# Performance work log

Hardware: AMD Instinct MI355X
Metric: run time of the kernel (lower is better)

## Reference

```python
import jax, jax.numpy as jnp
import numpy as np
from jax import lax

S, B, W = 128, 64, 16          # sent_len, batch, word_len
V, CV = 50000, 100             # word vocab, char vocab
WE, CE, FN, CK = 300, 30, 4, 3 # word emb dim, char emb dim, char filter num, char kernel
C = 512                        # cnn_out_channel
NT = 20                        # number of tags
NL = 3                         # number of GLU conv layers
PAD = 0


def setup_inputs() -> dict:
    key = jax.random.key(0)
    ks = jax.random.split(key, 16)
    words = jax.random.randint(ks[0], (S, B), 1, V)          # no pads -> full CRF mask
    chars = jax.random.randint(ks[1], (B, S, W), 1, CV)
    tags = jax.random.randint(ks[2], (S, B), 0, NT)
    word_emb = jax.random.normal(ks[3], (V, WE), jnp.float32) * 0.1
    char_emb = jax.random.normal(ks[4], (CV, CE), jnp.float32) * 0.1
    char_cnn_w = jax.random.normal(ks[5], (CE * FN, 1, CK), jnp.float32) * 0.1  # grouped conv, groups=CE
    char_cnn_b = jax.random.normal(ks[6], (CE * FN,), jnp.float32) * 0.01
    lin_w = jax.random.normal(ks[7], (WE + CE * FN, C), jnp.float32) * 0.05
    lin_b = jax.random.normal(ks[8], (C,), jnp.float32) * 0.01
    conv_w = jax.random.normal(ks[9], (NL, 2 * C, C, 3), jnp.float32) * 0.03
    conv_b = jax.random.normal(ks[10], (NL, 2 * C), jnp.float32) * 0.01
    fc_w = jax.random.normal(ks[11], (C, NT), jnp.float32) * 0.05
    fc_b = jax.random.normal(ks[12], (NT,), jnp.float32) * 0.01
    crf_start = jax.random.normal(ks[13], (NT,), jnp.float32) * 0.1
    crf_end = jax.random.normal(ks[14], (NT,), jnp.float32) * 0.1
    crf_trans = jax.random.normal(ks[15], (NT, NT), jnp.float32) * 0.1
    return dict(words=words, chars=chars, tags=tags, word_emb=word_emb, char_emb=char_emb,
                char_cnn_w=char_cnn_w, char_cnn_b=char_cnn_b, lin_w=lin_w, lin_b=lin_b,
                conv_w=conv_w, conv_b=conv_b, fc_w=fc_w, fc_b=fc_b,
                crf_start=crf_start, crf_end=crf_end, crf_trans=crf_trans)


def _emissions(words, chars, word_emb, char_emb, char_cnn_w, char_cnn_b,
               lin_w, lin_b, conv_w, conv_b, fc_w, fc_b):
    s, b = words.shape
    # word embeddings: [S,B,WE]
    emb_out = word_emb[words]
    # char embeddings + batched grouped char-CNN (replaces the python loop over sent positions)
    ch = char_emb[chars]                                   # [B,S,W,CE]
    ch = ch.reshape(b * s, W, CE).transpose(0, 2, 1)       # [B*S, CE, W]
    co = lax.conv_general_dilated(ch, char_cnn_w, (1,), 'VALID',
                                  dimension_numbers=('NCH', 'OIH', 'NCH'),
                                  feature_group_count=CE)
    co = co + char_cnn_b[None, :, None]                    # [B*S, CE*FN, W-CK+1]
    cf = co.max(axis=2).reshape(b, s, CE * FN).transpose(1, 0, 2)  # [S,B,120]
    word_features = jnp.concatenate([emb_out, cf], axis=2)  # [S,B,420]
    # gated-CNN (GLU) encoder
    h = word_features @ lin_w + lin_b                      # [S,B,C]
    h = jnp.transpose(h, (1, 2, 0))                        # [B,C,S]
    scale = jnp.sqrt(jnp.asarray(0.5, h.dtype))
    for l in range(conv_w.shape[0]):
        c = lax.conv_general_dilated(h, conv_w[l], (1,), ((1, 1),),
                                     dimension_numbers=('NCH', 'OIH', 'NCH'))
        c = c + conv_b[l][None, :, None]                   # [B,2C,S]
        a, g = jnp.split(c, 2, axis=1)
        h = (a * jax.nn.sigmoid(g) + h) * scale            # GLU + residual + scale
    enc = jnp.transpose(h, (2, 0, 1))                      # [S,B,C]
    emis = enc @ fc_w + fc_b                               # [S,B,NT]
    mask = (words != PAD)                                  # [S,B]
    return emis, mask


def _crf_nll(emis, tags, mask, crf_start, crf_end, crf_trans):
    s, b, nt = emis.shape
    maskf = mask.astype(emis.dtype)
    bi = jnp.arange(b)
    # numerator: score of the gold path
    emis_sc = jnp.take_along_axis(emis, tags[:, :, None], axis=2)[..., 0]  # [S,B]
    trans_sc = crf_trans[tags[:-1], tags[1:]]                              # [S-1,B]
    num = crf_start[tags[0]] + emis_sc[0] + ((trans_sc + emis_sc[1:]) * maskf[1:]).sum(0)
    last_idx = mask.sum(0).astype(jnp.int32) - 1
    num = num + crf_end[tags[last_idx, bi]]
    # denominator: forward algorithm (sequential DP over time)
    alpha0 = crf_start[None, :] + emis[0]                  # [B,NT]
    def step(alpha, xs):
        e_t, m_t = xs
        nxt = jax.nn.logsumexp(alpha[:, :, None] + crf_trans[None] + e_t[:, None, :], axis=1)
        return jnp.where(m_t[:, None], nxt, alpha), None
    alpha, _ = lax.scan(step, alpha0, (emis[1:], mask[1:]))
    logz = jax.nn.logsumexp(alpha + crf_end[None, :], axis=1)
    return -(num - logz).sum()


def _viterbi(emis, mask, crf_start, crf_end, crf_trans):
    s, b, nt = emis.shape
    bi = jnp.arange(b)
    ident = jnp.broadcast_to(jnp.arange(nt)[None, :], (b, nt))
    score0 = crf_start[None, :] + emis[0]                  # [B,NT]
    def step(score, xs):
        e_t, m_t = xs
        brd = score[:, :, None] + crf_trans[None]          # [B,NT_prev,NT_cur]
        bp = jnp.argmax(brd, axis=1)                       # [B,NT]
        nxt = jnp.max(brd, axis=1) + e_t
        score = jnp.where(m_t[:, None], nxt, score)
        bp = jnp.where(m_t[:, None], bp, ident)
        return score, bp
    final, bps = lax.scan(step, score0, (emis[1:], mask[1:]))  # bps [S-1,B,NT]
    last_tag = jnp.argmax(final + crf_end[None, :], axis=1)    # [B]
    def back(tag, bp):
        prev = bp[bi, tag]
        return prev, tag
    first_tag, rest = lax.scan(back, last_tag, bps, reverse=True)  # rest: tags at 1..S-1
    return jnp.concatenate([first_tag[None], rest], axis=0).astype(jnp.int32)  # [S,B]


def reference(words, chars, tags, word_emb, char_emb, char_cnn_w, char_cnn_b,
              lin_w, lin_b, conv_w, conv_b, fc_w, fc_b, crf_start, crf_end, crf_trans):
    emis, mask = _emissions(words, chars, word_emb, char_emb, char_cnn_w, char_cnn_b,
                            lin_w, lin_b, conv_w, conv_b, fc_w, fc_b)
    crf_out = _viterbi(emis, mask, crf_start, crf_end, crf_trans)
    crf_loss = _crf_nll(emis, tags, mask, crf_start, crf_end, crf_trans)
    return crf_out, crf_loss
```

## Files before the change

kernel.cpp:

```cpp
#include <hip/hip_runtime.h>
#include <math.h>

typedef unsigned short ushort_t;
typedef short bf16x8 __attribute__((ext_vector_type(8)));
typedef float f32x4 __attribute__((ext_vector_type(4)));
typedef unsigned short u16x8 __attribute__((ext_vector_type(8)));

#define S_ 128
#define B_ 64
#define W_ 16
#define CE_ 30
#define FN_ 4
#define WE_ 300
#define FEAT_ 420
#define C_ 512
#define NT_ 20
#define KL_ 448

#define LOG2E_ 1.44269504088896340736f
#define LN2_   0.69314718055994530942f

#define WF_OFF   0
#define EM_OFF   3440640
#define NLL_OFF  3604480
#define H0_OFF   3604608
#define HBUF_F   2129920
#define H1_OFF   (H0_OFF + HBUF_F)
#define WS_OFF   (H1_OFF + HBUF_F)
#define WSP_F    2359296
#define LW_OFF   (WS_OFF + WSP_F)
#define FS_OFF   (LW_OFF + 114688)
#define FW_OFF   (FS_OFF + 1835008)
#define WLAYER   (1024*1536)

__device__ __forceinline__ float b2f(ushort_t h) {
    unsigned u = ((unsigned)h) << 16;
    float f; __builtin_memcpy(&f, &u, 4); return f;
}
__device__ __forceinline__ ushort_t f2b(float f) {
    unsigned u; __builtin_memcpy(&u, &f, 4);
    unsigned r = (u + 0x7FFFu + ((u >> 16) & 1u)) >> 16;
    return (ushort_t)r;
}
__device__ __forceinline__ void gload16(const void* g, void* l) {
    __builtin_amdgcn_global_load_lds((const __attribute__((address_space(1))) void*)g,
                                     (__attribute__((address_space(3))) void*)l,
                                     16, 0, 0);
}

__global__ void k_word_gather(const int* __restrict__ words,
                              const float* __restrict__ word_emb,
                              float* __restrict__ wf) {
    int n = blockIdx.x;
    int wid = words[n];
    int t = threadIdx.x;
    if (t < WE_ / 4) {
        const float4* src = (const float4*)(word_emb + (size_t)wid * WE_);
        float4* dst = (float4*)(wf + (size_t)n * FEAT_);
        dst[t] = src[t];
    }
}

__global__ void k_char_cnn(const int* __restrict__ chars,
                           const float* __restrict__ char_emb,
                           const float* __restrict__ cw,
                           const float* __restrict__ cb,
                           float* __restrict__ wf) {
    int n = blockIdx.x;
    int b = n >> 7;
    int s = n & 127;
    __shared__ int cidx[W_];
    int t = threadIdx.x;
    if (t < W_) cidx[t] = chars[n * W_ + t];
    __syncthreads();
    if (t < CE_ * FN_) {
        int g = t >> 2;
        float w0 = cw[t*3+0], w1 = cw[t*3+1], w2 = cw[t*3+2];
        float x[W_];
        #pragma unroll
        for (int j = 0; j < W_; ++j) x[j] = char_emb[cidx[j] * CE_ + g];
        float m = -INFINITY;
        #pragma unroll
        for (int j = 0; j < W_ - 2; ++j) {
            float v = x[j]*w0 + x[j+1]*w1 + x[j+2]*w2;
            m = fmaxf(m, v);
        }
        wf[(size_t)(s * B_ + b) * FEAT_ + WE_ + t] = m + cb[t];
    }
}

__global__ void k_split_w(const float* __restrict__ conv_w,
                          ushort_t* __restrict__ Wt) {
    size_t i = (size_t)blockIdx.x * 256 + threadIdx.x;
    int ci = (int)(i & 511);
    int kr = (int)((i >> 9) % 3);
    size_t lo_ = i / 1536;
    Wt[i] = f2b(conv_w[lo_ * 1536 + (size_t)ci * 3 + kr]);
}

__global__ void k_split_lw(const float* __restrict__ lin_w,
                           ushort_t* __restrict__ Lh) {
    int k = blockIdx.x;
    int c = threadIdx.x;
    float v = (k < FEAT_) ? lin_w[(size_t)k * C_ + c] : 0.f;
    Lh[(size_t)c * KL_ + k] = f2b(v);
}

__global__ void k_split_wf(const float* __restrict__ wf,
                           ushort_t* __restrict__ Fh) {
    int np = blockIdx.x;
    int b = np >> 7, s = np & 127;
    const float* src = wf + (size_t)(s * B_ + b) * FEAT_;
    int t = threadIdx.x;
    #pragma unroll
    for (int r = 0; r < 2; ++r) {
        int k = t + r * 224;
        float v = (k < FEAT_) ? src[k] : 0.f;
        Fh[(size_t)np * KL_ + k] = f2b(v);
    }
}

__global__ void k_split_fw(const float* __restrict__ fc_w, float* __restrict__ fwT) {
    int idx = blockIdx.x * 256 + threadIdx.x;
    if (idx < NT_ * C_) {
        int j = idx >> 9, c = idx & 511;
        fwT[idx] = fc_w[(size_t)c * NT_ + j];
    }
}

__global__ void k_zero_pad(ushort_t* b0, ushort_t* b1) {
    ushort_t* buf = blockIdx.y ? b1 : b0;
    int b = blockIdx.x;
    int t = threadIdx.x;
    unsigned* r0 = (unsigned*)(buf + ((size_t)b * 130 + 0) * 512);
    unsigned* r1 = (unsigned*)(buf + ((size_t)b * 130 + 129) * 512);
    r0[t] = 0u; r1[t] = 0u;
}

__global__ __launch_bounds__(256) void k_lin_gemm(
    const ushort_t* __restrict__ Lh, const ushort_t* __restrict__ Fh,
    const float* __restrict__ lb, ushort_t* __restrict__ Oh)
{
    __shared__ short lds[8192];
    short* AhS = lds;
    short* BhS = lds + 4096;

    const int bid = blockIdx.x;
    const int c0 = (bid & 3) << 7;
    const int n0 = (bid >> 2) << 7;
    const int t = threadIdx.x;
    const int w = t >> 6;
    const int lane = t & 63;
    const int wr = w >> 1, wc = w & 1;

    const int srow0 = (w << 5) + (lane >> 2);
    const int srow1 = srow0 + 16;
    const int j0 = (lane & 3) ^ ((srow0 >> 1) & 3);
    const int j1 = (lane & 3) ^ ((srow1 >> 1) & 3);
    const size_t aoff0 = (size_t)(c0 + srow0) * KL_ + j0 * 8;
    const size_t aoff1 = (size_t)(c0 + srow1) * KL_ + j1 * 8;
    const size_t boff0 = (size_t)(n0 + srow0) * KL_ + j0 * 8;
    const size_t boff1 = (size_t)(n0 + srow1) * KL_ + j1 * 8;
    const int wofs = w << 10;

    const int lr = lane & 15, kg = lane >> 4;
    int aro[4], bro[4];
    #pragma unroll
    for (int m = 0; m < 4; ++m) { int r = (wr << 6) + (m << 4) + lr; aro[m] = (r << 5) + ((kg ^ ((r >> 1) & 3)) << 3); }
    #pragma unroll
    for (int n = 0; n < 4; ++n) { int r = (wc << 6) + (n << 4) + lr; bro[n] = (r << 5) + ((kg ^ ((r >> 1) & 3)) << 3); }

    f32x4 acc[4][4];
    #pragma unroll
    for (int m = 0; m < 4; ++m)
        #pragma unroll
        for (int n = 0; n < 4; ++n) acc[m][n] = (f32x4){0.f, 0.f, 0.f, 0.f};

    for (int k0 = 0; k0 < KL_; k0 += 32) {
        gload16(Lh + aoff0 + k0, AhS + wofs);
        gload16(Lh + aoff1 + k0, AhS + wofs + 512);
        gload16(Fh + boff0 + k0, BhS + wofs);
        gload16(Fh + boff1 + k0, BhS + wofs + 512);
        __syncthreads();
        bf16x8 avh[4], bvh[4];
        #pragma unroll
        for (int m = 0; m < 4; ++m) avh[m] = *(const bf16x8*)(AhS + aro[m]);
        #pragma unroll
        for (int n = 0; n < 4; ++n) bvh[n] = *(const bf16x8*)(BhS + bro[n]);
        #pragma unroll
        for (int m = 0; m < 4; ++m)
            #pragma unroll
            for (int n = 0; n < 4; ++n)
                acc[m][n] = __builtin_amdgcn_mfma_f32_16x16x32_bf16(avh[m], bvh[n], acc[m][n], 0, 0, 0);
        __syncthreads();
    }

    #pragma unroll
    for (int m = 0; m < 4; ++m) {
        const int c = c0 + (wr << 6) + (m << 4) + (kg << 2);
        float4 bb = *(const float4*)(lb + c);
        #pragma unroll
        for (int n = 0; n < 4; ++n) {
            const int np = n0 + (wc << 6) + (n << 4) + lr;
            const int b = np >> 7, s = np & 127;
            ushort4 h4;
            h4.x = f2b(acc[m][n][0] + bb.x);
            h4.y = f2b(acc[m][n][1] + bb.y);
            h4.z = f2b(acc[m][n][2] + bb.z);
            h4.w = f2b(acc[m][n][3] + bb.w);
            *(ushort4*)(Oh + ((size_t)b * 130 + s + 1) * 512 + c) = h4;
        }
    }
}

__global__ __launch_bounds__(256) void k_conv_gemm(
    const ushort_t* __restrict__ Wt, const ushort_t* __restrict__ Ht,
    const float* __restrict__ cb,
    ushort_t* __restrict__ Ot)
{
    __shared__ short lds[17408];
    short* AS = lds;
    short* BS = lds + 12288;
    float* g_lds = (float*)lds;

    const int bid  = blockIdx.x;
    const int co0  = (bid & 7) << 6;
    const int b    = bid >> 3;
    const int t    = threadIdx.x;
    const int w    = t >> 6;
    const int lane = t & 63;
    const int wr   = w >> 1;
    const int wc   = w & 1;

    const int srow0 = (w << 5) + (lane >> 2);
    const int srow1 = srow0 + 16;
    const int j0 = (lane & 3) ^ ((srow0 >> 1) & 3);
    const int j1 = (lane & 3) ^ ((srow1 >> 1) & 3);
    const int coA0 = (srow0 < 64) ? (co0 + srow0) : (512 + co0 + srow0 - 64);
    const int coA1 = (srow1 < 64) ? (co0 + srow1) : (512 + co0 + srow1 - 64);
    const size_t aoff0 = (size_t)coA0 * 1536 + j0 * 8;
    const size_t aoff1 = (size_t)coA1 * 1536 + j1 * 8;
    const int lrow = lane >> 2;
    const int wofs = w << 10;

    const int lr = lane & 15, kg = lane >> 4;
    int aro[4];
    #pragma unroll
    for (int m = 0; m < 4; ++m) { int r = (wr << 6) + (m << 4) + lr; aro[m] = (r << 5) + ((kg ^ ((r >> 1) & 3)) << 3); }
    int bro[3][4];
    #pragma unroll
    for (int kr = 0; kr < 3; ++kr)
        #pragma unroll
        for (int n = 0; n < 4; ++n) {
            int r = (wc << 6) + (n << 4) + lr + kr;
            bro[kr][n] = (r << 5) + ((kg ^ ((r >> 1) & 3)) << 3);
        }

    f32x4 acc[4][4];
    #pragma unroll
    for (int m = 0; m < 4; ++m)
        #pragma unroll
        for (int n = 0; n < 4; ++n) acc[m][n] = (f32x4){0.f, 0.f, 0.f, 0.f};

    for (int ci0 = 0; ci0 < 512; ci0 += 32) {
        #pragma unroll
        for (int kr = 0; kr < 3; ++kr) {
            gload16(Wt + aoff0 + kr * 512 + ci0, AS + kr * 4096 + wofs);
            gload16(Wt + aoff1 + kr * 512 + ci0, AS + kr * 4096 + wofs + 512);
        }
        for (int i = w; i < 9; i += 4) {
            const int rr = (i << 4) + lrow;
            const int sl = (lane & 3) ^ ((rr >> 1) & 3);
            gload16(Ht + ((size_t)b * 130 + rr) * 512 + ci0 + sl * 8, BS + (i << 9));
        }
        __syncthreads();
        #pragma unroll
        for (int kr = 0; kr < 3; ++kr) {
            const short* A_h = AS + kr * 4096;
            bf16x8 avh[4], bvh[4];
            #pragma unroll
            for (int m = 0; m < 4; ++m) avh[m] = *(const bf16x8*)(A_h + aro[m]);
            #pragma unroll
            for (int n = 0; n < 4; ++n) bvh[n] = *(const bf16x8*)(BS + bro[kr][n]);
            #pragma unroll
            for (int m = 0; m < 4; ++m)
                #pragma unroll
                for (int n = 0; n < 4; ++n)
                    acc[m][n] = __builtin_amdgcn_mfma_f32_16x16x32_bf16(avh[m], bvh[n], acc[m][n], 0, 0, 0);
        }
        __syncthreads();
    }

    const float rs = 0.70710678118654752f;
    if (wr == 1) {
        #pragma unroll
        for (int m = 0; m < 4; ++m) {
            const int co_l = (m << 4) + (kg << 2);
            float4 bg = *(const float4*)(cb + 512 + co0 + co_l);
            #pragma unroll
            for (int n = 0; n < 4; ++n) {
                const int s_l = (wc << 6) + (n << 4) + lr;
                float4 gv;
                gv.x = acc[m][n][0] + bg.x;
                gv.y = acc[m][n][1] + bg.y;
                gv.z = acc[m][n][2] + bg.z;
                gv.w = acc[m][n][3] + bg.w;
                *(float4*)&g_lds[s_l * 68 + co_l] = gv;
            }
        }
    }
    __syncthreads();
    if (wr == 0) {
        #pragma unroll
        for (int m = 0; m < 4; ++m) {
            const int co_l = (m << 4) + (kg << 2);
            float4 ba = *(const float4*)(cb + co0 + co_l);
            #pragma unroll
            for (int n = 0; n < 4; ++n) {
                const int s_l = (wc << 6) + (n << 4) + lr;
                float4 gv = *(const float4*)&g_lds[s_l * 68 + co_l];
                size_t dst = ((size_t)b * 130 + s_l + 1) * 512 + co0 + co_l;
                ushort4 rh = *(const ushort4*)(Ht + dst);
                float a0 = acc[m][n][0] + ba.x, g0 = gv.x;
                float a1 = acc[m][n][1] + ba.y, g1 = gv.y;
                float a2 = acc[m][n][2] + ba.z, g2 = gv.z;
                float a3 = acc[m][n][3] + ba.w, g3 = gv.w;
                ushort4 h4;
                h4.x = f2b((a0 / (1.f + expf(-g0)) + b2f(rh.x)) * rs);
                h4.y = f2b((a1 / (1.f + expf(-g1)) + b2f(rh.y)) * rs);
                h4.z = f2b((a2 / (1.f + expf(-g2)) + b2f(rh.z)) * rs);
                h4.w = f2b((a3 / (1.f + expf(-g3)) + b2f(rh.w)) * rs);
                *(ushort4*)(Ot + dst) = h4;
            }
        }
    }
}

__global__ __launch_bounds__(256) void k_emis3(const ushort_t* __restrict__ hh,
                                               const float* __restrict__ fwT,
                                               const float* __restrict__ fc_b,
                                               float* __restrict__ emis) {
    __shared__ short hlds[16 * 520];
    __shared__ float wlds[20 * 516];
    const int b  = blockIdx.y;
    const int sc = blockIdx.x;
    const int t  = threadIdx.x;
    const int w  = t >> 6, lane = t & 63;

    #pragma unroll
    for (int i = 0; i < 4; ++i) {
        int r = w * 4 + i;
        gload16(hh + ((size_t)b * 130 + sc * 16 + r + 1) * 512 + lane * 8,
                hlds + r * 520);
    }
    for (int idx = t; idx < 20 * 128; idx += 256) {
        int j = idx >> 7, cq = (idx & 127) << 2;
        *(float4*)&wlds[j * 516 + cq] = *(const float4*)(fwT + j * 512 + cq);
    }
    __syncthreads();

    #pragma unroll
    for (int pass = 0; pass < 2; ++pass) {
        int slot = t + pass * 256;
        if (slot < 16 * NT_) {
            int r = slot / NT_, j = slot - r * NT_;
            const short* hp = hlds + r * 520;
            const float* wp = wlds + j * 516;
            float acc = 0.f;
            for (int c0 = 0; c0 < 512; c0 += 8) {
                u16x8 hv = *(const u16x8*)(hp + c0);
                float4 w0 = *(const float4*)(wp + c0);
                float4 w1 = *(const float4*)(wp + c0 + 4);
                acc += b2f(hv[0])*w0.x + b2f(hv[1])*w0.y + b2f(hv[2])*w0.z + b2f(hv[3])*w0.w
                     + b2f(hv[4])*w1.x + b2f(hv[5])*w1.y + b2f(hv[6])*w1.z + b2f(hv[7])*w1.w;
            }
            int s = sc * 16 + r;
            emis[((size_t)s * B_ + b) * NT_ + j] = acc + fc_b[j];
        }
    }
}

#define VMAX(a, b) __builtin_elementwise_max((a), (b))
#define MAX20T(mx, a0, a1, a2, a3, a4) \
    { f32x4 mv_ = VMAX(VMAX(VMAX(a0, a1), VMAX(a2, a3)), a4); \
      mx = fmaxf(fmaxf(mv_[0], mv_[1]), fmaxf(mv_[2], mv_[3])); }
#define SEL(ov, oi, av, ai, bv2, bi2) \
    { bool g_ = (bv2) > (av); ov = g_ ? (bv2) : (av); oi = g_ ? (bi2) : (ai); }

__global__ __launch_bounds__(128) void k_crf(const float* __restrict__ emis,
                                             const int* __restrict__ words,
                                             const int* __restrict__ tags,
                                             const float* __restrict__ tstart,
                                             const float* __restrict__ tend,
                                             const float* __restrict__ ttrans,
                                             float* __restrict__ nll,
                                             float* __restrict__ out) {
    __shared__ float e_lds[S_ * NT_];
    __shared__ float pe_lds[S_ * NT_];
    __shared__ int   bp_lds[(S_ - 1) * NT_];
    __shared__ float alphaL[32];
    __shared__ float scoreL[32];
    const int b = blockIdx.x;
    const int t = threadIdx.x;

    for (int idx = t; idx < S_ * NT_; idx += 128) {
        int tt = idx / NT_, j = idx - tt * NT_;
        float ev = emis[((size_t)tt * B_ + b) * NT_ + j];
        e_lds[idx] = ev;
        pe_lds[idx] = __builtin_amdgcn_exp2f(ev * LOG2E_);
    }
    __syncthreads();

    const int ln = t & 63;
    unsigned long long mlo = __ballot(words[ln * B_ + b] != 0);
    unsigned long long mhi = __ballot(words[(64 + ln) * B_ + b] != 0);
    const bool act = ln < NT_;
    const int jc = act ? ln : 0;
    f32x4 t0, t1, t2, t3, t4;
    #define LDTC(v, q) v = (f32x4){ ttrans[(4*(q)+0)*NT_ + jc], ttrans[(4*(q)+1)*NT_ + jc], \
                                    ttrans[(4*(q)+2)*NT_ + jc], ttrans[(4*(q)+3)*NT_ + jc] }
    LDTC(t0, 0); LDTC(t1, 1); LDTC(t2, 2); LDTC(t3, 3); LDTC(t4, 4);

    if (t < 64) {
        float part = 0.f;
        for (int tt = ln; tt < S_; tt += 64) {
            int tgc = tags[tt * B_ + b];
            bool m = ((tt < 64 ? (mlo >> tt) : (mhi >> (tt - 64))) & 1ull) != 0;
            if (tt == 0) {
                part += tstart[tgc] + e_lds[tgc];
            } else if (m) {
                int tgp = tags[(tt - 1) * B_ + b];
                part += ttrans[tgp * NT_ + tgc] + e_lds[tt * NT_ + tgc];
            }
        }
        #pragma unroll
        for (int o = 32; o >= 1; o >>= 1) part += __shfl_down(part, o);

        f32x4 E0, E1, E2, E3, E4;
        #define EXPC(d, s) d[0]=__builtin_amdgcn_exp2f(s[0]*LOG2E_); d[1]=__builtin_amdgcn_exp2f(s[1]*LOG2E_); \
                           d[2]=__builtin_amdgcn_exp2f(s[2]*LOG2E_); d[3]=__builtin_amdgcn_exp2f(s[3]*LOG2E_)
        EXPC(E0, t0); EXPC(E1, t1); EXPC(E2, t2); EXPC(E3, t3); EXPC(E4, t4);

        float a0own = tstart[jc] + e_lds[jc];
        if (act) alphaL[ln] = a0own;
        asm volatile("s_waitcnt lgkmcnt(0)" ::: "memory");
        f32x4 a0 = *(const f32x4*)&alphaL[0];
        f32x4 a1 = *(const f32x4*)&alphaL[4];
        f32x4 a2 = *(const f32x4*)&alphaL[8];
        f32x4 a3 = *(const f32x4*)&alphaL[12];
        f32x4 a4 = *(const f32x4*)&alphaL[16];
        float m0; MAX20T(m0, a0, a1, a2, a3, a4);
        float beta = __builtin_amdgcn_exp2f((a0own - m0) * LOG2E_);
        int L2 = 0;
        for (int tt = 1; tt < S_; ++tt) {
            bool m = ((tt < 64 ? (mlo >> tt) : (mhi >> (tt - 64))) & 1ull) != 0;
            if (m) {
                float pe = pe_lds[tt * NT_ + jc];
                if (act) alphaL[ln] = beta;
                asm volatile("s_waitcnt lgkmcnt(0)" ::: "memory");
                f32x4 b0 = *(const f32x4*)&alphaL[0];
                f32x4 b1 = *(const f32x4*)&alphaL[4];
                f32x4 b2 = *(const f32x4*)&alphaL[8];
                f32x4 b3 = *(const f32x4*)&alphaL[12];
                f32x4 b4 = *(const f32x4*)&alphaL[16];
                float mx; MAX20T(mx, b0, b1, b2, b3, b4);
                f32x4 pr = b0 * E0 + b1 * E1 + b2 * E2 + b3 * E3 + b4 * E4;
                float dot = (pr[0] + pr[1]) + (pr[2] + pr[3]);
                unsigned bits; __builtin_memcpy(&bits, &mx, 4);
                int ex = (int)((bits >> 23) & 255u) - 127;
                unsigned rb = (unsigned)(127 - ex) << 23;
                float r; __builtin_memcpy(&r, &rb, 4);
                L2 += ex;
                beta = dot * r * pe;
            }
        }
        if (act) alphaL[ln] = beta;
        asm volatile("s_waitcnt lgkmcnt(0)" ::: "memory");
        f32x4 b0 = *(const f32x4*)&alphaL[0];
        f32x4 b1 = *(const f32x4*)&alphaL[4];
        f32x4 b2 = *(const f32x4*)&alphaL[8];
        f32x4 b3 = *(const f32x4*)&alphaL[12];
        f32x4 b4 = *(const f32x4*)&alphaL[16];
        #define LDE(v, q) v = (f32x4){ tend[4*(q)+0], tend[4*(q)+1], tend[4*(q)+2], tend[4*(q)+3] }
        f32x4 d0, d1, d2, d3, d4;
        LDE(d0, 0); LDE(d1, 1); LDE(d2, 2); LDE(d3, 3); LDE(d4, 4);
        f32x4 n0, n1, n2, n3, n4;
        EXPC(n0, d0); EXPC(n1, d1); EXPC(n2, d2); EXPC(n3, d3); EXPC(n4, d4);
        f32x4 pr = b0 * n0 + b1 * n1 + b2 * n2 + b3 * n3 + b4 * n4;
        float sm = (pr[0] + pr[1]) + (pr[2] + pr[3]);
        float logz = m0 + ((float)L2 + __builtin_amdgcn_logf(sm)) * LN2_;
        if (ln == 0) {
            int cnt = __popcll(mlo) + __popcll(mhi);
            float num = part + tend[tags[(cnt - 1) * B_ + b]];
            nll[b] = logz - num;
        }
    } else {
        float sown = tstart[jc] + e_lds[jc];
        if (act) scoreL[ln] = sown;
        asm volatile("s_waitcnt lgkmcnt(0)" ::: "memory");
        for (int tt = 1; tt < S_; ++tt) {
            float e = e_lds[tt * NT_ + jc];
            f32x4 a0 = *(const f32x4*)&scoreL[0];
            f32x4 a1 = *(const f32x4*)&scoreL[4];
            f32x4 a2 = *(const f32x4*)&scoreL[8];
            f32x4 a3 = *(const f32x4*)&scoreL[12];
            f32x4 a4 = *(const f32x4*)&scoreL[16];
            f32x4 v0 = a0 + t0, v1 = a1 + t1, v2 = a2 + t2, v3 = a3 + t3, v4 = a4 + t4;
            float p0v, p1v, p2v, p3v, p4v, p5v, p6v, p7v, p8v, p9v;
            int   p0i, p1i, p2i, p3i, p4i, p5i, p6i, p7i, p8i, p9i;
            SEL(p0v, p0i, v0[0], 0,  v0[1], 1);
            SEL(p1v, p1i, v0[2], 2,  v0[3], 3);
            SEL(p2v, p2i, v1[0], 4,  v1[1], 5);
            SEL(p3v, p3i, v1[2], 6,  v1[3], 7);
            SEL(p4v, p4i, v2[0], 8,  v2[1], 9);
            SEL(p5v, p5i, v2[2], 10, v2[3], 11);
            SEL(p6v, p6i, v3[0], 12, v3[1], 13);
            SEL(p7v, p7i, v3[2], 14, v3[3], 15);
            SEL(p8v, p8i, v4[0], 16, v4[1], 17);
            SEL(p9v, p9i, v4[2], 18, v4[3], 19);
            float q0v, q1v, q2v, q3v, q4v; int q0i, q1i, q2i, q3i, q4i;
            SEL(q0v, q0i, p0v, p0i, p1v, p1i);
            SEL(q1v, q1i, p2v, p2i, p3v, p3i);
            SEL(q2v, q2i, p4v, p4i, p5v, p5i);
            SEL(q3v, q3i, p6v, p6i, p7v, p7i);
            SEL(q4v, q4i, p8v, p8i, p9v, p9i);
            float r0v, r1v; int r0i, r1i;
            SEL(r0v, r0i, q0v, q0i, q1v, q1i);
            SEL(r1v, r1i, q2v, q2i, q3v, q3i);
            float s0v; int s0i;
            SEL(s0v, s0i, r0v, r0i, r1v, r1i);
            float best; int bi;
            SEL(best, bi, s0v, s0i, q4v, q4i);
            bool m = ((tt < 64 ? (mlo >> tt) : (mhi >> (tt - 64))) & 1ull) != 0;
            float nxt = best + e;
            sown = m ? nxt : sown;
            if (act) {
                scoreL[ln] = sown;
                bp_lds[(tt - 1) * NT_ + ln] = m ? bi : ln;
            }
            asm volatile("s_waitcnt lgkmcnt(0)" ::: "memory");
        }
        if (ln == 0) {
            f32x4 a0 = *(const f32x4*)&scoreL[0];
            f32x4 a1 = *(const f32x4*)&scoreL[4];
            f32x4 a2 = *(const f32x4*)&scoreL[8];
            f32x4 a3 = *(const f32x4*)&scoreL[12];
            f32x4 a4 = *(const f32x4*)&scoreL[16];
            f32x4 d0 = (f32x4){ tend[0],  tend[1],  tend[2],  tend[3]  };
            f32x4 d1 = (f32x4){ tend[4],  tend[5],  tend[6],  tend[7]  };
            f32x4 d2 = (f32x4){ tend[8],  tend[9],  tend[10], tend[11] };
            f32x4 d3 = (f32x4){ tend[12], tend[13], tend[14], tend[15] };
            f32x4 d4 = (f32x4){ tend[16], tend[17], tend[18], tend[19] };
            f32x4 v0 = a0 + d0, v1 = a1 + d1, v2 = a2 + d2, v3 = a3 + d3, v4 = a4 + d4;
            float p0v, p1v, p2v, p3v, p4v, p5v, p6v, p7v, p8v, p9v;
            int   p0i, p1i, p2i, p3i, p4i, p5i, p6i, p7i, p8i, p9i;
            SEL(p0v, p0i, v0[0], 0,  v0[1], 1);
            SEL(p1v, p1i, v0[2], 2,  v0[3], 3);
            SEL(p2v, p2i, v1[0], 4,  v1[1], 5);
            SEL(p3v, p3i, v1[2], 6,  v1[3], 7);
            SEL(p4v, p4i, v2[0], 8,  v2[1], 9);
            SEL(p5v, p5i, v2[2], 10, v2[3], 11);
            SEL(p6v, p6i, v3[0], 12, v3[1], 13);
            SEL(p7v, p7i, v3[2], 14, v3[3], 15);
            SEL(p8v, p8i, v4[0], 16, v4[1], 17);
            SEL(p9v, p9i, v4[2], 18, v4[3], 19);
            float q0v, q1v, q2v, q3v, q4v; int q0i, q1i, q2i, q3i, q4i;
            SEL(q0v, q0i, p0v, p0i, p1v, p1i);
            SEL(q1v, q1i, p2v, p2i, p3v, p3i);
            SEL(q2v, q2i, p4v, p4i, p5v, p5i);
            SEL(q3v, q3i, p6v, p6i, p7v, p7i);
            SEL(q4v, q4i, p8v, p8i, p9v, p9i);
            float r0v, r1v; int r0i, r1i;
            SEL(r0v, r0i, q0v, q0i, q1v, q1i);
            SEL(r1v, r1i, q2v, q2i, q3v, q3i);
            float s0v; int s0i;
            SEL(s0v, s0i, r0v, r0i, r1v, r1i);
            float best; int bt;
            SEL(best, bt, s0v, s0i, q4v, q4i);
            int tag = bt;
            for (int tt = S_ - 1; tt >= 1; --tt) {
                out[tt * B_ + b] = (float)tag;
                tag = bp_lds[(tt - 1) * NT_ + tag];
            }
            out[b] = (float)tag;
        }
    }
}

__global__ void k_loss(const float* __restrict__ nll, float* __restrict__ out) {
    float v = nll[threadIdx.x];
    #pragma unroll
    for (int o = 32; o >= 1; o >>= 1) v += __shfl_down(v, o);
    if (threadIdx.x == 0) out[S_ * B_] = v;
}

extern "C" void kernel_launch(void* const* d_in, const int* in_sizes, int n_in,
                              void* d_out, int out_size, void* d_ws, size_t ws_size,
                              hipStream_t stream) {
    (void)in_sizes; (void)n_in; (void)out_size; (void)ws_size;
    const int*   words     = (const int*)d_in[0];
    const int*   chars     = (const int*)d_in[1];
    const int*   tags      = (const int*)d_in[2];
    const float* word_emb  = (const float*)d_in[3];
    const float* char_emb  = (const float*)d_in[4];
    const float* ccw       = (const float*)d_in[5];
    const float* ccb       = (const float*)d_in[6];
    const float* lin_w     = (const float*)d_in[7];
    const float* lin_b     = (const float*)d_in[8];
    const float* conv_w    = (const float*)d_in[9];
    const float* conv_b    = (const float*)d_in[10];
    const float* fc_w      = (const float*)d_in[11];
    const float* fc_b      = (const float*)d_in[12];
    const float* crf_start = (const float*)d_in[13];
    const float* crf_end   = (const float*)d_in[14];
    const float* crf_trans = (const float*)d_in[15];

    float* ws   = (float*)d_ws;
    float* wf   = ws + WF_OFF;
    float* em   = ws + EM_OFF;
    float* nll  = ws + NLL_OFF;
    ushort_t* h0  = (ushort_t*)(ws + H0_OFF);
    ushort_t* h1  = (ushort_t*)(ws + H1_OFF);
    ushort_t* wsp = (ushort_t*)(ws + WS_OFF);
    ushort_t* lwp = (ushort_t*)(ws + LW_OFF);
    ushort_t* fsp = (ushort_t*)(ws + FS_OFF);
    float* fwT  = ws + FW_OFF;
    float* out  = (float*)d_out;

    k_word_gather<<<S_ * B_, 128, 0, stream>>>(words, word_emb, wf);
    k_char_cnn<<<B_ * S_, 128, 0, stream>>>(chars, char_emb, ccw, ccb, wf);
    k_split_w<<<18432, 256, 0, stream>>>(conv_w, wsp);
    k_split_lw<<<KL_, 512, 0, stream>>>(lin_w, lwp);
    k_split_wf<<<S_ * B_, 224, 0, stream>>>(wf, fsp);
    k_split_fw<<<40, 256, 0, stream>>>(fc_w, fwT);
    k_lin_gemm<<<256, 256, 0, stream>>>(lwp, fsp, lin_b, h0);
    k_zero_pad<<<dim3(64, 2), 256, 0, stream>>>(h0, h1);

    k_conv_gemm<<<512, 256, 0, stream>>>(wsp,              h0, conv_b,        h1);
    k_conv_gemm<<<512, 256, 0, stream>>>(wsp + WLAYER,     h1, conv_b + 1024, h0);
    k_conv_gemm<<<512, 256, 0, stream>>>(wsp + 2*WLAYER,   h0, conv_b + 2048, h1);

    k_emis3<<<dim3(8, B_), 256, 0, stream>>>(h1, fwT, fc_b, em);
    k_crf<<<B_, 128, 0, stream>>>(em, words, tags, crf_start, crf_end, crf_trans, nll, out);
    k_loss<<<1, 64, 0, stream>>>(nll, out);
}
```

Before: 217.0 us.

## Split CRF forward and Viterbi recursions into bidirectional halves meeting at midpoint

The CRF kernel now runs four wavefronts per batch element. Forward-alpha and Viterbi-forward cover steps 1..63, while a backward-beta recursion and a backward Viterbi cover steps 127..63. The partition function is combined from the forward and backward vectors at the midpoint, and the Viterbi path is traced outward from the best midpoint tag in both directions. This roughly halves the serial dependency chain length, which was the latency bottleneck, at the cost of more LDS and numerically different log-sum ordering and tie-breaking.

```diff
diff --git a/kernel.cpp b/kernel.cpp
--- a/kernel.cpp
+++ b/kernel.cpp
@@ -386,8 +386,28 @@
       mx = fmaxf(fmaxf(mv_[0], mv_[1]), fmaxf(mv_[2], mv_[3])); }
 #define SEL(ov, oi, av, ai, bv2, bi2) \
     { bool g_ = (bv2) > (av); ov = g_ ? (bv2) : (av); oi = g_ ? (bi2) : (ai); }
-
-__global__ __launch_bounds__(128) void k_crf(const float* __restrict__ emis,
+#define ARGMAX20(best, bi, v0, v1, v2, v3, v4) \
+    { float p0v,p1v,p2v,p3v,p4v,p5v,p6v,p7v,p8v,p9v; \
+      int   p0i,p1i,p2i,p3i,p4i,p5i,p6i,p7i,p8i,p9i; \
+      SEL(p0v,p0i, v0[0],0,  v0[1],1);  SEL(p1v,p1i, v0[2],2,  v0[3],3); \
+      SEL(p2v,p2i, v1[0],4,  v1[1],5);  SEL(p3v,p3i, v1[2],6,  v1[3],7); \
+      SEL(p4v,p4i, v2[0],8,  v2[1],9);  SEL(p5v,p5i, v2[2],10, v2[3],11); \
+      SEL(p6v,p6i, v3[0],12, v3[1],13); SEL(p7v,p7i, v3[2],14, v3[3],15); \
+      SEL(p8v,p8i, v4[0],16, v4[1],17); SEL(p9v,p9i, v4[2],18, v4[3],19); \
+      float q0v,q1v,q2v,q3v,q4v; int q0i,q1i,q2i,q3i,q4i; \
+      SEL(q0v,q0i,p0v,p0i,p1v,p1i); SEL(q1v,q1i,p2v,p2i,p3v,p3i); \
+      SEL(q2v,q2i,p4v,p4i,p5v,p5i); SEL(q3v,q3i,p6v,p6i,p7v,p7i); \
+      SEL(q4v,q4i,p8v,p8i,p9v,p9i); \
+      float r0v,r1v; int r0i,r1i; \
+      SEL(r0v,r0i,q0v,q0i,q1v,q1i); SEL(r1v,r1i,q2v,q2i,q3v,q3i); \
+      float s0v; int s0i; \
+      SEL(s0v,s0i,r0v,r0i,r1v,r1i); \
+      SEL(best,bi,s0v,s0i,q4v,q4i); }
+#define EXPC(d, s) d[0]=__builtin_amdgcn_exp2f(s[0]*LOG2E_); d[1]=__builtin_amdgcn_exp2f(s[1]*LOG2E_); \
+                   d[2]=__builtin_amdgcn_exp2f(s[2]*LOG2E_); d[3]=__builtin_amdgcn_exp2f(s[3]*LOG2E_)
+#define LGKM0() asm volatile("s_waitcnt lgkmcnt(0)" ::: "memory")
+
+__global__ __launch_bounds__(256) void k_crf(const float* __restrict__ emis,
                                              const int* __restrict__ words,
                                              const int* __restrict__ tags,
                                              const float* __restrict__ tstart,
@@ -397,13 +417,17 @@
                                              float* __restrict__ out) {
     __shared__ float e_lds[S_ * NT_];
     __shared__ float pe_lds[S_ * NT_];
-    __shared__ int   bp_lds[(S_ - 1) * NT_];
-    __shared__ float alphaL[32];
-    __shared__ float scoreL[32];
+    __shared__ int   P_lds[S_ * NT_];
+    __shared__ float brA[32], brB[32], brC[32], brD[32];
+    __shared__ float Fv[NT_], Gv[NT_], a63[NT_], g63[NT_];
+    __shared__ float CfL, CbL;
+    __shared__ int tag63L;
     const int b = blockIdx.x;
     const int t = threadIdx.x;
-
-    for (int idx = t; idx < S_ * NT_; idx += 128) {
+    const int w = t >> 6;
+    const int ln = t & 63;
+
+    for (int idx = t; idx < S_ * NT_; idx += 256) {
         int tt = idx / NT_, j = idx - tt * NT_;
         float ev = emis[((size_t)tt * B_ + b) * NT_ + j];
         e_lds[idx] = ev;
@@ -411,21 +435,18 @@
     }
     __syncthreads();
 
-    const int ln = t & 63;
     unsigned long long mlo = __ballot(words[ln * B_ + b] != 0);
     unsigned long long mhi = __ballot(words[(64 + ln) * B_ + b] != 0);
     const bool act = ln < NT_;
     const int jc = act ? ln : 0;
-    f32x4 t0, t1, t2, t3, t4;
-    #define LDTC(v, q) v = (f32x4){ ttrans[(4*(q)+0)*NT_ + jc], ttrans[(4*(q)+1)*NT_ + jc], \
-                                    ttrans[(4*(q)+2)*NT_ + jc], ttrans[(4*(q)+3)*NT_ + jc] }
-    LDTC(t0, 0); LDTC(t1, 1); LDTC(t2, 2); LDTC(t3, 3); LDTC(t4, 4);
-
-    if (t < 64) {
-        float part = 0.f;
+    float part = 0.f;
+
+    #define MBIT(tt) ((((tt) < 64 ? (mlo >> (tt)) : (mhi >> ((tt) - 64))) & 1ull) != 0)
+
+    if (w == 0) {
         for (int tt = ln; tt < S_; tt += 64) {
             int tgc = tags[tt * B_ + b];
-            bool m = ((tt < 64 ? (mlo >> tt) : (mhi >> (tt - 64))) & 1ull) != 0;
+            bool m = MBIT(tt);
             if (tt == 0) {
                 part += tstart[tgc] + e_lds[tgc];
             } else if (m) {
@@ -436,33 +457,34 @@
         #pragma unroll
         for (int o = 32; o >= 1; o >>= 1) part += __shfl_down(part, o);
 
+        f32x4 t0, t1, t2, t3, t4;
+        #define LDTC(v, q) v = (f32x4){ ttrans[(4*(q)+0)*NT_ + jc], ttrans[(4*(q)+1)*NT_ + jc], \
+                                        ttrans[(4*(q)+2)*NT_ + jc], ttrans[(4*(q)+3)*NT_ + jc] }
+        LDTC(t0, 0); LDTC(t1, 1); LDTC(t2, 2); LDTC(t3, 3); LDTC(t4, 4);
         f32x4 E0, E1, E2, E3, E4;
-        #define EXPC(d, s) d[0]=__builtin_amdgcn_exp2f(s[0]*LOG2E_); d[1]=__builtin_amdgcn_exp2f(s[1]*LOG2E_); \
-                           d[2]=__builtin_amdgcn_exp2f(s[2]*LOG2E_); d[3]=__builtin_amdgcn_exp2f(s[3]*LOG2E_)
         EXPC(E0, t0); EXPC(E1, t1); EXPC(E2, t2); EXPC(E3, t3); EXPC(E4, t4);
 
         float a0own = tstart[jc] + e_lds[jc];
-        if (act) alphaL[ln] = a0own;
-        asm volatile("s_waitcnt lgkmcnt(0)" ::: "memory");
-        f32x4 a0 = *(const f32x4*)&alphaL[0];
-        f32x4 a1 = *(const f32x4*)&alphaL[4];
-        f32x4 a2 = *(const f32x4*)&alphaL[8];
-        f32x4 a3 = *(const f32x4*)&alphaL[12];
-        f32x4 a4 = *(const f32x4*)&alphaL[16];
+        if (act) brA[ln] = a0own;
+        LGKM0();
+        f32x4 a0 = *(const f32x4*)&brA[0];
+        f32x4 a1 = *(const f32x4*)&brA[4];
+        f32x4 a2 = *(const f32x4*)&brA[8];
+        f32x4 a3 = *(const f32x4*)&brA[12];
+        f32x4 a4 = *(const f32x4*)&brA[16];
         float m0; MAX20T(m0, a0, a1, a2, a3, a4);
         float beta = __builtin_amdgcn_exp2f((a0own - m0) * LOG2E_);
         int L2 = 0;
-        for (int tt = 1; tt < S_; ++tt) {
-            bool m = ((tt < 64 ? (mlo >> tt) : (mhi >> (tt - 64))) & 1ull) != 0;
-            if (m) {
+        for (int tt = 1; tt < 64; ++tt) {
+            if (MBIT(tt)) {
                 float pe = pe_lds[tt * NT_ + jc];
-                if (act) alphaL[ln] = beta;
-                asm volatile("s_waitcnt lgkmcnt(0)" ::: "memory");
-                f32x4 b0 = *(const f32x4*)&alphaL[0];
-                f32x4 b1 = *(const f32x4*)&alphaL[4];
-                f32x4 b2 = *(const f32x4*)&alphaL[8];
-                f32x4 b3 = *(const f32x4*)&alphaL[12];
-                f32x4 b4 = *(const f32x4*)&alphaL[16];
+                if (act) brA[ln] = beta;
+                LGKM0();
+                f32x4 b0 = *(const f32x4*)&brA[0];
+                f32x4 b1 = *(const f32x4*)&brA[4];
+                f32x4 b2 = *(const f32x4*)&brA[8];
+                f32x4 b3 = *(const f32x4*)&brA[12];
+                f32x4 b4 = *(const f32x4*)&brA[16];
                 float mx; MAX20T(mx, b0, b1, b2, b3, b4);
                 f32x4 pr = b0 * E0 + b1 * E1 + b2 * E2 + b3 * E3 + b4 * E4;
                 float dot = (pr[0] + pr[1]) + (pr[2] + pr[3]);
@@ -474,115 +496,130 @@
                 beta = dot * r * pe;
             }
         }
-        if (act) alphaL[ln] = beta;
-        asm volatile("s_waitcnt lgkmcnt(0)" ::: "memory");
-        f32x4 b0 = *(const f32x4*)&alphaL[0];
-        f32x4 b1 = *(const f32x4*)&alphaL[4];
-        f32x4 b2 = *(const f32x4*)&alphaL[8];
-        f32x4 b3 = *(const f32x4*)&alphaL[12];
-        f32x4 b4 = *(const f32x4*)&alphaL[16];
-        #define LDE(v, q) v = (f32x4){ tend[4*(q)+0], tend[4*(q)+1], tend[4*(q)+2], tend[4*(q)+3] }
-        f32x4 d0, d1, d2, d3, d4;
-        LDE(d0, 0); LDE(d1, 1); LDE(d2, 2); LDE(d3, 3); LDE(d4, 4);
-        f32x4 n0, n1, n2, n3, n4;
-        EXPC(n0, d0); EXPC(n1, d1); EXPC(n2, d2); EXPC(n3, d3); EXPC(n4, d4);
-        f32x4 pr = b0 * n0 + b1 * n1 + b2 * n2 + b3 * n3 + b4 * n4;
-        float sm = (pr[0] + pr[1]) + (pr[2] + pr[3]);
-        float logz = m0 + ((float)L2 + __builtin_amdgcn_logf(sm)) * LN2_;
-        if (ln == 0) {
-            int cnt = __popcll(mlo) + __popcll(mhi);
-            float num = part + tend[tags[(cnt - 1) * B_ + b]];
-            nll[b] = logz - num;
-        }
-    } else {
+        if (act) Fv[ln] = beta;
+        if (ln == 0) CfL = m0 + (float)L2 * LN2_;
+    } else if (w == 1) {
+        f32x4 r0, r1, r2, r3, r4;
+        #define LDTR(v, q) v = (f32x4){ ttrans[jc*NT_ + 4*(q)+0], ttrans[jc*NT_ + 4*(q)+1], \
+                                        ttrans[jc*NT_ + 4*(q)+2], ttrans[jc*NT_ + 4*(q)+3] }
+        LDTR(r0, 0); LDTR(r1, 1); LDTR(r2, 2); LDTR(r3, 3); LDTR(r4, 4);
+        f32x4 E0, E1, E2, E3, E4;
+        EXPC(E0, r0); EXPC(E1, r1); EXPC(E2, r2); EXPC(E3, r3); EXPC(E4, r4);
+        f32x4 d0 = (f32x4){ tend[0],  tend[1],  tend[2],  tend[3]  };
+        f32x4 d1 = (f32x4){ tend[4],  tend[5],  tend[6],  tend[7]  };
+        f32x4 d2 = (f32x4){ tend[8],  tend[9],  tend[10], tend[11] };
+        f32x4 d3 = (f32x4){ tend[12], tend[13], tend[14], tend[15] };
+        f32x4 d4 = (f32x4){ tend[16], tend[17], tend[18], tend[19] };
+        float mend; MAX20T(mend, d0, d1, d2, d3, d4);
+        float G = __builtin_amdgcn_exp2f((tend[jc] - mend) * LOG2E_);
+        int L2b = 0;
+        for (int tt = 126; tt >= 63; --tt) {
+            if (MBIT(tt + 1)) {
+                float w_own = G * pe_lds[(tt + 1) * NT_ + jc];
+                if (act) brB[ln] = w_own;
+                LGKM0();
+                f32x4 q0 = *(const f32x4*)&brB[0];
+                f32x4 q1 = *(const f32x4*)&brB[4];
+                f32x4 q2 = *(const f32x4*)&brB[8];
+                f32x4 q3 = *(const f32x4*)&brB[12];
+                f32x4 q4 = *(const f32x4*)&brB[16];
+                float mx; MAX20T(mx, q0, q1, q2, q3, q4);
+                f32x4 pr = q0 * E0 + q1 * E1 + q2 * E2 + q3 * E3 + q4 * E4;
+                float dot = (pr[0] + pr[1]) + (pr[2] + pr[3]);
+                unsigned bits; __builtin_memcpy(&bits, &mx, 4);
+                int ex = (int)((bits >> 23) & 255u) - 127;
+                unsigned rb = (unsigned)(127 - ex) << 23;
+                float r; __builtin_memcpy(&r, &rb, 4);
+                L2b += ex;
+                G = dot * r;
+            }
+        }
+        if (act) Gv[ln] = G;
+        if (ln == 0) CbL = mend + (float)L2b * LN2_;
+    } else if (w == 2) {
+        f32x4 t0, t1, t2, t3, t4;
+        LDTC(t0, 0); LDTC(t1, 1); LDTC(t2, 2); LDTC(t3, 3); LDTC(t4, 4);
         float sown = tstart[jc] + e_lds[jc];
-        if (act) scoreL[ln] = sown;
-        asm volatile("s_waitcnt lgkmcnt(0)" ::: "memory");
-        for (int tt = 1; tt < S_; ++tt) {
+        if (act) brC[ln] = sown;
+        LGKM0();
+        for (int tt = 1; tt < 64; ++tt) {
             float e = e_lds[tt * NT_ + jc];
-            f32x4 a0 = *(const f32x4*)&scoreL[0];
-            f32x4 a1 = *(const f32x4*)&scoreL[4];
-            f32x4 a2 = *(const f32x4*)&scoreL[8];
-            f32x4 a3 = *(const f32x4*)&scoreL[12];
-            f32x4 a4 = *(const f32x4*)&scoreL[16];
+            f32x4 a0 = *(const f32x4*)&brC[0];
+            f32x4 a1 = *(const f32x4*)&brC[4];
+            f32x4 a2 = *(const f32x4*)&brC[8];
+            f32x4 a3 = *(const f32x4*)&brC[12];
+            f32x4 a4 = *(const f32x4*)&brC[16];
             f32x4 v0 = a0 + t0, v1 = a1 + t1, v2 = a2 + t2, v3 = a3 + t3, v4 = a4 + t4;
-            float p0v, p1v, p2v, p3v, p4v, p5v, p6v, p7v, p8v, p9v;
-            int   p0i, p1i, p2i, p3i, p4i, p5i, p6i, p7i, p8i, p9i;
-            SEL(p0v, p0i, v0[0], 0,  v0[1], 1);
-            SEL(p1v, p1i, v0[2], 2,  v0[3], 3);
-            SEL(p2v, p2i, v1[0], 4,  v1[1], 5);
-            SEL(p3v, p3i, v1[2], 6,  v1[3], 7);
-            SEL(p4v, p4i, v2[0], 8,  v2[1], 9);
-            SEL(p5v, p5i, v2[2], 10, v2[3], 11);
-            SEL(p6v, p6i, v3[0], 12, v3[1], 13);
-            SEL(p7v, p7i, v3[2], 14, v3[3], 15);
-            SEL(p8v, p8i, v4[0], 16, v4[1], 17);
-            SEL(p9v, p9i, v4[2], 18, v4[3], 19);
-            float q0v, q1v, q2v, q3v, q4v; int q0i, q1i, q2i, q3i, q4i;
-            SEL(q0v, q0i, p0v, p0i, p1v, p1i);
-            SEL(q1v, q1i, p2v, p2i, p3v, p3i);
-            SEL(q2v, q2i, p4v, p4i, p5v, p5i);
-            SEL(q3v, q3i, p6v, p6i, p7v, p7i);
-            SEL(q4v, q4i, p8v, p8i, p9v, p9i);
-            float r0v, r1v; int r0i, r1i;
-            SEL(r0v, r0i, q0v, q0i, q1v, q1i);
-            SEL(r1v, r1i, q2v, q2i, q3v, q3i);
-            float s0v; int s0i;
-            SEL(s0v, s0i, r0v, r0i, r1v, r1i);
             float best; int bi;
-            SEL(best, bi, s0v, s0i, q4v, q4i);
-            bool m = ((tt < 64 ? (mlo >> tt) : (mhi >> (tt - 64))) & 1ull) != 0;
+            ARGMAX20(best, bi, v0, v1, v2, v3, v4);
+            bool m = MBIT(tt);
             float nxt = best + e;
             sown = m ? nxt : sown;
             if (act) {
-                scoreL[ln] = sown;
-                bp_lds[(tt - 1) * NT_ + ln] = m ? bi : ln;
-            }
-            asm volatile("s_waitcnt lgkmcnt(0)" ::: "memory");
-        }
-        if (ln == 0) {
-            f32x4 a0 = *(const f32x4*)&scoreL[0];
-            f32x4 a1 = *(const f32x4*)&scoreL[4];
-            f32x4 a2 = *(const f32x4*)&scoreL[8];
-            f32x4 a3 = *(const f32x4*)&scoreL[12];
-            f32x4 a4 = *(const f32x4*)&scoreL[16];
-            f32x4 d0 = (f32x4){ tend[0],  tend[1],  tend[2],  tend[3]  };
-            f32x4 d1 = (f32x4){ tend[4],  tend[5],  tend[6],  tend[7]  };
-            f32x4 d2 = (f32x4){ tend[8],  tend[9],  tend[10], tend[11] };
-            f32x4 d3 = (f32x4){ tend[12], tend[13], tend[14], tend[15] };
-            f32x4 d4 = (f32x4){ tend[16], tend[17], tend[18], tend[19] };
-            f32x4 v0 = a0 + d0, v1 = a1 + d1, v2 = a2 + d2, v3 = a3 + d3, v4 = a4 + d4;
-            float p0v, p1v, p2v, p3v, p4v, p5v, p6v, p7v, p8v, p9v;
-            int   p0i, p1i, p2i, p3i, p4i, p5i, p6i, p7i, p8i, p9i;
-            SEL(p0v, p0i, v0[0], 0,  v0[1], 1);
-            SEL(p1v, p1i, v0[2], 2,  v0[3], 3);
-            SEL(p2v, p2i, v1[0], 4,  v1[1], 5);
-            SEL(p3v, p3i, v1[2], 6,  v1[3], 7);
-            SEL(p4v, p4i, v2[0], 8,  v2[1], 9);
-            SEL(p5v, p5i, v2[2], 10, v2[3], 11);
-            SEL(p6v, p6i, v3[0], 12, v3[1], 13);
-            SEL(p7v, p7i, v3[2], 14, v3[3], 15);
-            SEL(p8v, p8i, v4[0], 16, v4[1], 17);
-            SEL(p9v, p9i, v4[2], 18, v4[3], 19);
-            float q0v, q1v, q2v, q3v, q4v; int q0i, q1i, q2i, q3i, q4i;
-            SEL(q0v, q0i, p0v, p0i, p1v, p1i);
-            SEL(q1v, q1i, p2v, p2i, p3v, p3i);
-            SEL(q2v, q2i, p4v, p4i, p5v, p5i);
-            SEL(q3v, q3i, p6v, p6i, p7v, p7i);
-            SEL(q4v, q4i, p8v, p8i, p9v, p9i);
-            float r0v, r1v; int r0i, r1i;
-            SEL(r0v, r0i, q0v, q0i, q1v, q1i);
-            SEL(r1v, r1i, q2v, q2i, q3v, q3i);
-            float s0v; int s0i;
-            SEL(s0v, s0i, r0v, r0i, r1v, r1i);
-            float best; int bt;
-            SEL(best, bt, s0v, s0i, q4v, q4i);
-            int tag = bt;
-            for (int tt = S_ - 1; tt >= 1; --tt) {
-                out[tt * B_ + b] = (float)tag;
-                tag = bp_lds[(tt - 1) * NT_ + tag];
-            }
-            out[b] = (float)tag;
+                brC[ln] = sown;
+                P_lds[tt * NT_ + ln] = m ? bi : ln;
+            }
+            LGKM0();
+        }
+        if (act) a63[ln] = sown;
+    } else {
+        f32x4 r0, r1, r2, r3, r4;
+        LDTR(r0, 0); LDTR(r1, 1); LDTR(r2, 2); LDTR(r3, 3); LDTR(r4, 4);
+        float gown = tend[jc];
+        if (act) brD[ln] = gown + e_lds[127 * NT_ + jc];
+        LGKM0();
+        for (int tt = 126; tt >= 63; --tt) {
+            f32x4 q0 = *(const f32x4*)&brD[0];
+            f32x4 q1 = *(const f32x4*)&brD[4];
+            f32x4 q2 = *(const f32x4*)&brD[8];
+            f32x4 q3 = *(const f32x4*)&brD[12];
+            f32x4 q4 = *(const f32x4*)&brD[16];
+            f32x4 v0 = r0 + q0, v1 = r1 + q1, v2 = r2 + q2, v3 = r3 + q3, v4 = r4 + q4;
+            float best; int bi;
+            ARGMAX20(best, bi, v0, v1, v2, v3, v4);
+            bool m = MBIT(tt + 1);
+            gown = m ? best : gown;
+            if (act) {
+                P_lds[(tt + 1) * NT_ + ln] = m ? bi : ln;
+                brD[ln] = gown + e_lds[tt * NT_ + jc];
+            }
+            LGKM0();
+        }
+        if (act) g63[ln] = gown;
+    }
+    __syncthreads();
+
+    if (t == 0) {
+        float zf = 0.f;
+        #pragma unroll
+        for (int j = 0; j < NT_; ++j) zf += Fv[j] * Gv[j];
+        float logz = CfL + CbL + __builtin_amdgcn_logf(zf) * LN2_;
+        int cnt = __popcll(mlo) + __popcll(mhi);
+        float num = part + tend[tags[(cnt - 1) * B_ + b]];
+        nll[b] = logz - num;
+        float bv = a63[0] + g63[0]; int bt = 0;
+        #pragma unroll
+        for (int j = 1; j < NT_; ++j) {
+            float v = a63[j] + g63[j];
+            if (v > bv) { bv = v; bt = j; }
+        }
+        tag63L = bt;
+    }
+    __syncthreads();
+
+    if (t == 128) {
+        int tag = tag63L;
+        out[63 * B_ + b] = (float)tag;
+        for (int tt = 63; tt >= 1; --tt) {
+            tag = P_lds[tt * NT_ + tag];
+            out[(tt - 1) * B_ + b] = (float)tag;
+        }
+    }
+    if (t == 192) {
+        int tag = tag63L;
+        for (int tt = 64; tt < 128; ++tt) {
+            tag = P_lds[tt * NT_ + tag];
+            out[tt * B_ + b] = (float)tag;
         }
     }
 }
@@ -641,6 +678,6 @@
     k_conv_gemm<<<512, 256, 0, stream>>>(wsp + 2*WLAYER,   h0, conv_b + 2048, h1);
 
     k_emis3<<<dim3(8, B_), 256, 0, stream>>>(h1, fwT, fc_b, em);
-    k_crf<<<B_, 128, 0, stream>>>(em, words, tags, crf_start, crf_end, crf_trans, nll, out);
+    k_crf<<<B_, 256, 0, stream>>>(em, words, tags, crf_start, crf_end, crf_trans, nll, out);
     k_loss<<<1, 64, 0, stream>>>(nll, out);
 }
```

New measurement: 192.6 us. -11.2%, faster.
